# Kernel optimization log

Measured on AMD Instinct MI355X. Metric: run time of the kernel, lower is better.

Reference implementation:

```python
import math
import jax, jax.numpy as jnp
import numpy as np

B, S, H, NH = 4, 2048, 1024, 16
HD = H // NH
SCALE = math.sqrt(H)  # module divides by sqrt(hidden_dim), not sqrt(head_dim)


def setup_inputs() -> dict:
    key = jax.random.key(0)
    ks = jax.random.split(key, 9)
    lim = 1.0 / math.sqrt(H)
    def lin(kw, kb):
        W = jax.random.uniform(kw, (H, H), jnp.float32, -lim, lim)
        b = jax.random.uniform(kb, (H,), jnp.float32, -lim, lim)
        return W, b
    Wq, bq = lin(ks[0], ks[1])
    Wk, bk = lin(ks[2], ks[3])
    Wv, bv = lin(ks[4], ks[5])
    Wo, bo = lin(ks[6], ks[7])
    hidden_states = jax.random.normal(ks[8], (B, S, H), jnp.float32)
    masks = jnp.ones((B, S), jnp.float32)
    return {"hidden_states": hidden_states, "masks": masks,
            "Wq": Wq, "bq": bq, "Wk": Wk, "bk": bk,
            "Wv": Wv, "bv": bv, "Wo": Wo, "bo": bo}


def reference(hidden_states, masks, Wq, bq, Wk, bk, Wv, bv, Wo, bo):
    bsz, msl, hdim = hidden_states.shape
    def proj(W, b):
        # [b, s, h] -> [b, nh, s, hd]
        y = hidden_states @ W.T + b
        return y.reshape(bsz, msl, NH, HD).transpose(0, 2, 1, 3)
    q = proj(Wq, bq)
    k = proj(Wk, bk)
    v = proj(Wv, bv)
    scores = jnp.einsum('bnqd,bnkd->bnqk', q, k) / SCALE
    # mask outer product: [b,1,q,k], zero where either token is padded
    m2 = (masks[:, None, :, None] * masks[:, None, None, :])
    scores = jnp.where(m2 == 0, jnp.float32(-1e12), scores)
    attn = jax.nn.softmax(scores, axis=-1)
    ctx = jnp.einsum('bnqk,bnkd->bnqd', attn, v)
    ctx = ctx.transpose(0, 2, 1, 3).reshape(bsz, msl, hdim)
    return ctx @ Wo.T + bo
```

## Files before the change

kernel.cpp:

```cpp
#include <hip/hip_runtime.h>
#include <hip/hip_bf16.h>
#include <stdint.h>

typedef unsigned short u16;
typedef __attribute__((ext_vector_type(4))) float f32x4;
typedef __attribute__((ext_vector_type(8))) short bf16x8;
typedef __attribute__((ext_vector_type(4))) unsigned int u32x4;

#define GLL16(src, dst) __builtin_amdgcn_global_load_lds( \
    (const __attribute__((address_space(1))) void*)(src), \
    (__attribute__((address_space(3))) void*)(dst), 16, 0, 0)

static __device__ __forceinline__ u16 f2bf(float x) {
    uint32_t u = __builtin_bit_cast(uint32_t, x);
    u += 0x7fffu + ((u >> 16) & 1u);
    return (u16)(u >> 16);
}

static __device__ __forceinline__ uint32_t cvtpk(float lo, float hi) {
    uint32_t r;
    asm("v_cvt_pk_bf16_f32 %0, %1, %2" : "=v"(r) : "v"(lo), "v"(hi));
    return r;
}

__global__ __launch_bounds__(256) void cvt_f32_bf16(
        const float* __restrict__ in, u16* __restrict__ out, int n4) {
    int i = blockIdx.x * 256 + threadIdx.x;
    if (i >= n4) return;
    float4 v = ((const float4*)in)[i];
    ushort4 o;
    o.x = f2bf(v.x); o.y = f2bf(v.y); o.z = f2bf(v.z); o.w = f2bf(v.w);
    ((ushort4*)out)[i] = o;
}

__global__ __launch_bounds__(256) void cvt_w4(
        const float* __restrict__ s0, const float* __restrict__ s1,
        const float* __restrict__ s2, const float* __restrict__ s3,
        u16* __restrict__ dst) {
    int wsel = blockIdx.y;
    const float* s = (wsel == 0) ? s0 : (wsel == 1) ? s1 : (wsel == 2) ? s2 : s3;
    int i = blockIdx.x * 256 + threadIdx.x;
    float4 v = ((const float4*)s)[i];
    ushort4 o;
    o.x = f2bf(v.x); o.y = f2bf(v.y); o.z = f2bf(v.z); o.w = f2bf(v.w);
    ((ushort4*)(dst + (size_t)wsel * 1024 * 1024))[i] = o;
}

__global__ __launch_bounds__(256, 2) void gemm_qkv(
        const u16* __restrict__ A, const u16* __restrict__ W,
        const float* __restrict__ bq, const float* __restrict__ bk,
        const float* __restrict__ bv,
        u16* __restrict__ Qo, u16* __restrict__ Ko, u16* __restrict__ Vo) {
    __shared__ __align__(16) u16 As[2][128 * 32];
    __shared__ __align__(16) u16 Bs[2][128 * 32];
    const int tid = threadIdx.x;
    const int lane = tid & 63;
    const int w = tid >> 6, wm = w >> 1, wn = w & 1;
    const int l15 = lane & 15, l4 = lane >> 4;
    int v = (blockIdx.x & 7) * 192 + (blockIdx.x >> 3);
    int vy = v / 24, vx = v - vy * 24;
    const int m0 = vy * 128, n0 = vx * 128;

    f32x4 acc[4][4];
#pragma unroll
    for (int i = 0; i < 4; i++)
#pragma unroll
        for (int j = 0; j < 4; j++) acc[i][j] = f32x4{0.f, 0.f, 0.f, 0.f};

#define QKV_STAGE(buf, kt) do {                                            \
    _Pragma("unroll")                                                      \
    for (int i_ = 0; i_ < 2; i_++) {                                       \
        int c_ = tid + i_ * 256;                                           \
        int row_ = c_ >> 2, slot_ = c_ & 3;                                \
        int cc_ = slot_ ^ ((row_ >> 1) & 3);                               \
        GLL16(A + (size_t)(m0 + row_) * 1024 + (kt) + cc_ * 8, As[buf] + c_ * 8); \
    }                                                                      \
    _Pragma("unroll")                                                      \
    for (int i_ = 0; i_ < 2; i_++) {                                       \
        int c_ = tid + i_ * 256;                                           \
        int row_ = c_ >> 2, slot_ = c_ & 3;                                \
        int cc_ = slot_ ^ ((row_ >> 1) & 3);                               \
        GLL16(W + (size_t)(n0 + row_) * 1024 + (kt) + cc_ * 8, Bs[buf] + c_ * 8); \
    }                                                                      \
} while (0)

    QKV_STAGE(0, 0);
    __syncthreads();

    for (int kt = 0; kt < 1024; kt += 32) {
        const int cur = (kt >> 5) & 1;
        if (kt != 992) QKV_STAGE(cur ^ 1, kt + 32);

        bf16x8 af[4], bfr[4];
#pragma unroll
        for (int i = 0; i < 4; i++) {
            int row = wm * 64 + i * 16 + l15;
            int slot = l4 ^ ((row >> 1) & 3);
            af[i] = *(const bf16x8*)(As[cur] + row * 32 + slot * 8);
        }
#pragma unroll
        for (int j = 0; j < 4; j++) {
            int row = wn * 64 + j * 16 + l15;
            int slot = l4 ^ ((row >> 1) & 3);
            bfr[j] = *(const bf16x8*)(Bs[cur] + row * 32 + slot * 8);
        }
#pragma unroll
        for (int i = 0; i < 4; i++)
#pragma unroll
            for (int j = 0; j < 4; j++)
                acc[i][j] = __builtin_amdgcn_mfma_f32_16x16x32_bf16(af[i], bfr[j], acc[i][j], 0, 0, 0);
        __syncthreads();
    }
#undef QKV_STAGE

#pragma unroll
    for (int j = 0; j < 4; j++) {
        int col = n0 + wn * 64 + j * 16 + l15;
        int sel = col >> 10;
        float bvv = (sel == 0) ? bq[col] : (sel == 1) ? bk[col - 1024] : bv[col - 2048];
#pragma unroll
        for (int i = 0; i < 4; i++) {
            int rowb = m0 + wm * 64 + i * 16 + l4 * 4;
            if (sel == 0) {
#pragma unroll
                for (int r = 0; r < 4; r++)
                    Qo[(size_t)(rowb + r) * 1024 + col] = f2bf(acc[i][j][r] + bvv);
            } else if (sel == 1) {
#pragma unroll
                for (int r = 0; r < 4; r++)
                    Ko[(size_t)(rowb + r) * 1024 + (col - 1024)] = f2bf(acc[i][j][r] + bvv);
            } else {
                int cc = col - 2048;
                int bb = rowb >> 11;
                int sp = ((m0 + wm * 64) & 2047) + (i >> 1) * 32 + l4 * 8 + (i & 1) * 4;
                int hh = cc >> 6, dd = cc & 63;
                ushort4 o;
                o.x = f2bf(acc[i][j][0] + bvv);
                o.y = f2bf(acc[i][j][1] + bvv);
                o.z = f2bf(acc[i][j][2] + bvv);
                o.w = f2bf(acc[i][j][3] + bvv);
                *(ushort4*)(Vo + ((size_t)((bb * 16 + hh) * 64 + dd)) * 2048 + sp) = o;
            }
        }
    }
}

__global__ __launch_bounds__(256, 2) void gemm_o(
        const u16* __restrict__ A, const u16* __restrict__ W,
        const float* __restrict__ bias, float* __restrict__ out) {
    __shared__ __align__(16) u16 As[2][128 * 32];
    __shared__ __align__(16) u16 Bs[2][128 * 32];
    const int tid = threadIdx.x;
    const int lane = tid & 63;
    const int w = tid >> 6, wm = w >> 1, wn = w & 1;
    const int l15 = lane & 15, l4 = lane >> 4;
    int v = (blockIdx.x & 7) * 64 + (blockIdx.x >> 3);
    int vy = v >> 3, vx = v & 7;
    const int m0 = vy * 128, n0 = vx * 128;

    f32x4 acc[4][4];
#pragma unroll
    for (int i = 0; i < 4; i++)
#pragma unroll
        for (int j = 0; j < 4; j++) acc[i][j] = f32x4{0.f, 0.f, 0.f, 0.f};

#define O_STAGE(buf, kt) do {                                              \
    _Pragma("unroll")                                                      \
    for (int i_ = 0; i_ < 2; i_++) {                                       \
        int c_ = tid + i_ * 256;                                           \
        int row_ = c_ >> 2, slot_ = c_ & 3;                                \
        int cc_ = slot_ ^ ((row_ >> 1) & 3);                               \
        GLL16(A + (size_t)(m0 + row_) * 1024 + (kt) + cc_ * 8, As[buf] + c_ * 8); \
    }                                                                      \
    _Pragma("unroll")                                                      \
    for (int i_ = 0; i_ < 2; i_++) {                                       \
        int c_ = tid + i_ * 256;                                           \
        int row_ = c_ >> 2, slot_ = c_ & 3;                                \
        int cc_ = slot_ ^ ((row_ >> 1) & 3);                               \
        GLL16(W + (size_t)(n0 + row_) * 1024 + (kt) + cc_ * 8, Bs[buf] + c_ * 8); \
    }                                                                      \
} while (0)

    O_STAGE(0, 0);
    __syncthreads();

    for (int kt = 0; kt < 1024; kt += 32) {
        const int cur = (kt >> 5) & 1;
        if (kt != 992) O_STAGE(cur ^ 1, kt + 32);

        bf16x8 af[4], bfr[4];
#pragma unroll
        for (int i = 0; i < 4; i++) {
            int row = wm * 64 + i * 16 + l15;
            int slot = l4 ^ ((row >> 1) & 3);
            af[i] = *(const bf16x8*)(As[cur] + row * 32 + slot * 8);
        }
#pragma unroll
        for (int j = 0; j < 4; j++) {
            int row = wn * 64 + j * 16 + l15;
            int slot = l4 ^ ((row >> 1) & 3);
            bfr[j] = *(const bf16x8*)(Bs[cur] + row * 32 + slot * 8);
        }
#pragma unroll
        for (int i = 0; i < 4; i++)
#pragma unroll
            for (int j = 0; j < 4; j++)
                acc[i][j] = __builtin_amdgcn_mfma_f32_16x16x32_bf16(af[i], bfr[j], acc[i][j], 0, 0, 0);
        __syncthreads();
    }
#undef O_STAGE

#pragma unroll
    for (int j = 0; j < 4; j++) {
        int col = n0 + wn * 64 + j * 16 + l15;
        float bvv = bias[col];
#pragma unroll
        for (int i = 0; i < 4; i++) {
            int rowb = m0 + wm * 64 + i * 16 + l4 * 4;
#pragma unroll
            for (int r = 0; r < 4; r++)
                out[(size_t)(rowb + r) * 1024 + col] = acc[i][j][r] + bvv;
        }
    }
}

__global__ __launch_bounds__(256, 3) void attn_fused(
        const u16* __restrict__ Q, const u16* __restrict__ K,
        const u16* __restrict__ Vt, const float* __restrict__ mask,
        u16* __restrict__ ctx) {
    __shared__ __align__(16) u16 Ks[2][64 * 64];
    __shared__ __align__(16) u16 Vs[2][64 * 64];
    __shared__ int mflag[4];

    const int tid = threadIdx.x, lane = tid & 63, w = tid >> 6;
    const int l15 = lane & 15, l4 = lane >> 4;
    const int bid = blockIdx.x;
    const int inner = bid >> 3;
    const int bh = ((inner >> 4) << 3) | (bid & 7);
    const int b = bh >> 4, h = bh & 15;
    const int qw = (inner & 15) * 128 + w * 32;
    const float SC2 = 0.03125f * 1.44269504088896f;
    const float THR2 = 8.0f;

    const u16* Qg = Q + (size_t)b * 2048 * 1024 + h * 64;
    const u16* Kg = K + (size_t)b * 2048 * 1024 + h * 64;
    const u16* Vg = Vt + (size_t)bh * 64 * 2048;
    const float* mp = mask + b * 2048;

    {
        float4 a = ((const float4*)mp)[tid * 2];
        float4 c = ((const float4*)mp)[tid * 2 + 1];
        bool bad = (a.x == 0.f) | (a.y == 0.f) | (a.z == 0.f) | (a.w == 0.f) |
                   (c.x == 0.f) | (c.y == 0.f) | (c.z == 0.f) | (c.w == 0.f);
        unsigned long long bal = __ballot(bad);
        if (lane == 0) mflag[w] = (bal != 0ull);
    }

    bf16x8 qfr[2][2];
#pragma unroll
    for (int qi = 0; qi < 2; qi++)
#pragma unroll
        for (int kf = 0; kf < 2; kf++)
            qfr[qi][kf] = *(const bf16x8*)(Qg + (size_t)(qw + qi * 16 + l15) * 1024 + kf * 32 + l4 * 8);

    float mqs[2];
#pragma unroll
    for (int qi = 0; qi < 2; qi++)
        mqs[qi] = (mp[qw + qi * 16 + l15] != 0.f) ? SC2 : 0.f;

    __syncthreads();
    const bool anym = (mflag[0] | mflag[1] | mflag[2] | mflag[3]) != 0;

#define STAGE_KV(buf, kvbase) do {                                         \
    _Pragma("unroll")                                                      \
    for (int i_ = 0; i_ < 2; i_++) {                                       \
        int c_ = tid + i_ * 256;                                           \
        int row_ = c_ >> 3, slot_ = c_ & 7;                                \
        int cc_ = slot_ ^ (row_ & 7);                                      \
        GLL16(Kg + (size_t)((kvbase) + row_) * 1024 + cc_ * 8, Ks[buf] + c_ * 8); \
    }                                                                      \
    _Pragma("unroll")                                                      \
    for (int i_ = 0; i_ < 2; i_++) {                                       \
        int c_ = tid + i_ * 256;                                           \
        int row_ = c_ >> 3, slot_ = c_ & 7;                                \
        int cc_ = slot_ ^ (row_ & 7);                                      \
        GLL16(Vg + (size_t)row_ * 2048 + (kvbase) + cc_ * 8, Vs[buf] + c_ * 8); \
    }                                                                      \
} while (0)

    float m_run[2] = {0.f, 0.f};
    f32x4 acc_l[2];
    f32x4 oaccT[4][2];
#pragma unroll
    for (int qi = 0; qi < 2; qi++) acc_l[qi] = f32x4{0.f, 0.f, 0.f, 0.f};
#pragma unroll
    for (int df = 0; df < 4; df++)
#pragma unroll
        for (int qi = 0; qi < 2; qi++) oaccT[df][qi] = f32x4{0.f, 0.f, 0.f, 0.f};

    const u32x4 ones4 = u32x4{0x3F803F80u, 0x3F803F80u, 0x3F803F80u, 0x3F803F80u};
    const bf16x8 ones = __builtin_bit_cast(bf16x8, ones4);

    STAGE_KV(0, 0);
    __syncthreads();

    for (int it = 0; it < 32; ++it) {
        const int cur = it & 1;
        const int kv0 = it * 64;

        if (it != 31) STAGE_KV(cur ^ 1, kv0 + 64);

        bf16x8 kfr[4][2];
#pragma unroll
        for (int kvf = 0; kvf < 4; kvf++)
#pragma unroll
            for (int kf = 0; kf < 2; kf++) {
                int row = kvf * 16 + l15;
                int slot = (kf * 4 + l4) ^ (row & 7);
                kfr[kvf][kf] = *(const bf16x8*)(Ks[cur] + row * 64 + slot * 8);
            }
        f32x4 p[4][2];
#pragma unroll
        for (int kvf = 0; kvf < 4; kvf++)
#pragma unroll
            for (int qi = 0; qi < 2; qi++) p[kvf][qi] = f32x4{0.f, 0.f, 0.f, 0.f};
        __builtin_amdgcn_s_setprio(1);
#pragma unroll
        for (int kvf = 0; kvf < 4; kvf++)
#pragma unroll
            for (int qi = 0; qi < 2; qi++)
#pragma unroll
                for (int kf = 0; kf < 2; kf++)
                    p[kvf][qi] = __builtin_amdgcn_mfma_f32_16x16x32_bf16(kfr[kvf][kf], qfr[qi][kf], p[kvf][qi], 0, 0, 0);
        __builtin_amdgcn_s_setprio(0);

        if (!anym) {
#pragma unroll
            for (int qi = 0; qi < 2; qi++) {
                float mneg = -m_run[qi];
#pragma unroll
                for (int kvf = 0; kvf < 4; kvf++)
#pragma unroll
                    for (int r = 0; r < 4; r++)
                        p[kvf][qi][r] = __builtin_fmaf(p[kvf][qi][r], mqs[qi], mneg);
            }
        } else {
            float4 mkv[4];
#pragma unroll
            for (int kvf = 0; kvf < 4; kvf++)
                mkv[kvf] = ((const float4*)(mp + kv0))[kvf * 4 + l4];
#pragma unroll
            for (int qi = 0; qi < 2; qi++) {
                float mneg = -m_run[qi];
#pragma unroll
                for (int kvf = 0; kvf < 4; kvf++)
#pragma unroll
                    for (int r = 0; r < 4; r++) {
                        float bb = (mkv[kvf][r] != 0.f) ? mneg : -1e12f;
                        p[kvf][qi][r] = __builtin_fmaf(p[kvf][qi][r], mqs[qi], bb);
                    }
            }
        }

        float d2[2];
#pragma unroll
        for (int qi = 0; qi < 2; qi++) {
            float a0 = fmaxf(fmaxf(p[0][qi][0], p[0][qi][1]), fmaxf(p[0][qi][2], p[0][qi][3]));
            float a1 = fmaxf(fmaxf(p[1][qi][0], p[1][qi][1]), fmaxf(p[1][qi][2], p[1][qi][3]));
            float a2 = fmaxf(fmaxf(p[2][qi][0], p[2][qi][1]), fmaxf(p[2][qi][2], p[2][qi][3]));
            float a3 = fmaxf(fmaxf(p[3][qi][0], p[3][qi][1]), fmaxf(p[3][qi][2], p[3][qi][3]));
            float t = fmaxf(fmaxf(a0, a1), fmaxf(a2, a3));
            t = fmaxf(t, __shfl_xor(t, 16));
            t = fmaxf(t, __shfl_xor(t, 32));
            d2[qi] = t;
        }
        if (!__all((d2[0] <= THR2) && (d2[1] <= THR2))) {
#pragma unroll
            for (int qi = 0; qi < 2; qi++) {
                float dd = fmaxf(d2[qi], 0.f);
                float sc = __builtin_amdgcn_exp2f(-dd);
                m_run[qi] += dd;
                acc_l[qi] *= sc;
#pragma unroll
                for (int df = 0; df < 4; df++) oaccT[df][qi] *= sc;
#pragma unroll
                for (int kvf = 0; kvf < 4; kvf++)
#pragma unroll
                    for (int r = 0; r < 4; r++) p[kvf][qi][r] -= dd;
            }
        }
#pragma unroll
        for (int qi = 0; qi < 2; qi++)
#pragma unroll
            for (int kvf = 0; kvf < 4; kvf++)
#pragma unroll
                for (int r = 0; r < 4; r++)
                    p[kvf][qi][r] = __builtin_amdgcn_exp2f(p[kvf][qi][r]);

        bf16x8 pb[2][2];
#pragma unroll
        for (int qi = 0; qi < 2; qi++)
#pragma unroll
            for (int kf = 0; kf < 2; kf++) {
                u32x4 t;
                t.x = cvtpk(p[2 * kf][qi][0], p[2 * kf][qi][1]);
                t.y = cvtpk(p[2 * kf][qi][2], p[2 * kf][qi][3]);
                t.z = cvtpk(p[2 * kf + 1][qi][0], p[2 * kf + 1][qi][1]);
                t.w = cvtpk(p[2 * kf + 1][qi][2], p[2 * kf + 1][qi][3]);
                pb[qi][kf] = __builtin_bit_cast(bf16x8, t);
            }

        bf16x8 vfr[4][2];
#pragma unroll
        for (int df = 0; df < 4; df++)
#pragma unroll
            for (int kf = 0; kf < 2; kf++) {
                int row = df * 16 + l15;
                int slot = (kf * 4 + l4) ^ (row & 7);
                vfr[df][kf] = *(const bf16x8*)(Vs[cur] + row * 64 + slot * 8);
            }

        __builtin_amdgcn_s_setprio(1);
#pragma unroll
        for (int df = 0; df < 4; df++)
#pragma unroll
            for (int qi = 0; qi < 2; qi++)
#pragma unroll
                for (int kf = 0; kf < 2; kf++)
                    oaccT[df][qi] = __builtin_amdgcn_mfma_f32_16x16x32_bf16(vfr[df][kf], pb[qi][kf], oaccT[df][qi], 0, 0, 0);
#pragma unroll
        for (int qi = 0; qi < 2; qi++)
#pragma unroll
            for (int kf = 0; kf < 2; kf++)
                acc_l[qi] = __builtin_amdgcn_mfma_f32_16x16x32_bf16(ones, pb[qi][kf], acc_l[qi], 0, 0, 0);
        __builtin_amdgcn_s_setprio(0);

        __syncthreads();
    }

#pragma unroll
    for (int qi = 0; qi < 2; qi++) {
        float rl = 1.0f / acc_l[qi][0];
        int tok = qw + qi * 16 + l15;
#pragma unroll
        for (int df = 0; df < 4; df++) {
            uint2 o;
            o.x = cvtpk(oaccT[df][qi][0] * rl, oaccT[df][qi][1] * rl);
            o.y = cvtpk(oaccT[df][qi][2] * rl, oaccT[df][qi][3] * rl);
            *(uint2*)(ctx + (size_t)(b * 2048 + tok) * 1024 + h * 64 + df * 16 + l4 * 4) = o;
        }
    }
#undef STAGE_KV
}

extern "C" void kernel_launch(void* const* d_in, const int* in_sizes, int n_in,
                              void* d_out, int out_size, void* d_ws, size_t ws_size,
                              hipStream_t stream) {
    const float* hs    = (const float*)d_in[0];
    const float* masks = (const float*)d_in[1];
    const float* Wq = (const float*)d_in[2];
    const float* bq = (const float*)d_in[3];
    const float* Wk = (const float*)d_in[4];
    const float* bk = (const float*)d_in[5];
    const float* Wv = (const float*)d_in[6];
    const float* bv = (const float*)d_in[7];
    const float* Wo = (const float*)d_in[8];
    const float* bo = (const float*)d_in[9];

    const int NT = 4 * 2048;
    const int H = 1024;

    u16* hs_b = (u16*)d_ws;
    u16* w_b  = hs_b + (size_t)NT * H;
    u16* wo_b = w_b + (size_t)3 * H * H;
    u16* Qb   = w_b + (size_t)4 * H * H;
    u16* Kb   = Qb + (size_t)NT * H;
    u16* Vtb  = Kb + (size_t)NT * H;
    u16* Cb   = hs_b;

    cvt_f32_bf16<<<NT * H / 1024, 256, 0, stream>>>(hs, hs_b, NT * H / 4);
    cvt_w4<<<dim3(H * H / 1024, 4), 256, 0, stream>>>(Wq, Wk, Wv, Wo, w_b);

    gemm_qkv<<<1536, 256, 0, stream>>>(hs_b, w_b, bq, bk, bv, Qb, Kb, Vtb);

    attn_fused<<<1024, 256, 0, stream>>>(Qb, Kb, Vtb, masks, Cb);

    gemm_o<<<512, 256, 0, stream>>>(Cb, wo_b, bo, (float*)d_out);
}
```

Before: 202.4 us.

## Load K/V fragments directly from global memory, dropping LDS staging and barriers

Removes the double-buffered LDS staging of K and V tiles and the per-iteration __syncthreads. Each wave now reads its K and V MFMA fragments straight from global memory, relying on L2 and cache reuse across the four waves. The mask check becomes per-wave with no barrier, and the max-reduction shuffles are deferred into the rare rescale branch. The trade is four times the global/L2 traffic per block, with load latency no longer hidden by an async prefetch of the next tile. The gain is no LDS use, no block-wide syncs and possibly higher occupancy.

```diff
diff --git a/kernel.cpp b/kernel.cpp
--- a/kernel.cpp
+++ b/kernel.cpp
@@ -228,10 +228,6 @@
         const u16* __restrict__ Q, const u16* __restrict__ K,
         const u16* __restrict__ Vt, const float* __restrict__ mask,
         u16* __restrict__ ctx) {
-    __shared__ __align__(16) u16 Ks[2][64 * 64];
-    __shared__ __align__(16) u16 Vs[2][64 * 64];
-    __shared__ int mflag[4];
-
     const int tid = threadIdx.x, lane = tid & 63, w = tid >> 6;
     const int l15 = lane & 15, l4 = lane >> 4;
     const int bid = blockIdx.x;
@@ -247,13 +243,15 @@
     const u16* Vg = Vt + (size_t)bh * 64 * 2048;
     const float* mp = mask + b * 2048;
 
+    bool anym;
     {
-        float4 a = ((const float4*)mp)[tid * 2];
-        float4 c = ((const float4*)mp)[tid * 2 + 1];
-        bool bad = (a.x == 0.f) | (a.y == 0.f) | (a.z == 0.f) | (a.w == 0.f) |
-                   (c.x == 0.f) | (c.y == 0.f) | (c.z == 0.f) | (c.w == 0.f);
-        unsigned long long bal = __ballot(bad);
-        if (lane == 0) mflag[w] = (bal != 0ull);
+        bool bad = false;
+#pragma unroll
+        for (int i = 0; i < 8; i++) {
+            float4 a = ((const float4*)mp)[lane * 8 + i];
+            bad |= (a.x == 0.f) | (a.y == 0.f) | (a.z == 0.f) | (a.w == 0.f);
+        }
+        anym = (__ballot(bad) != 0ull);
     }
 
     bf16x8 qfr[2][2];
@@ -267,26 +265,6 @@
 #pragma unroll
     for (int qi = 0; qi < 2; qi++)
         mqs[qi] = (mp[qw + qi * 16 + l15] != 0.f) ? SC2 : 0.f;
-
-    __syncthreads();
-    const bool anym = (mflag[0] | mflag[1] | mflag[2] | mflag[3]) != 0;
-
-#define STAGE_KV(buf, kvbase) do {                                         \
-    _Pragma("unroll")                                                      \
-    for (int i_ = 0; i_ < 2; i_++) {                                       \
-        int c_ = tid + i_ * 256;                                           \
-        int row_ = c_ >> 3, slot_ = c_ & 7;                                \
-        int cc_ = slot_ ^ (row_ & 7);                                      \
-        GLL16(Kg + (size_t)((kvbase) + row_) * 1024 + cc_ * 8, Ks[buf] + c_ * 8); \
-    }                                                                      \
-    _Pragma("unroll")                                                      \
-    for (int i_ = 0; i_ < 2; i_++) {                                       \
-        int c_ = tid + i_ * 256;                                           \
-        int row_ = c_ >> 3, slot_ = c_ & 7;                                \
-        int cc_ = slot_ ^ (row_ & 7);                                      \
-        GLL16(Vg + (size_t)row_ * 2048 + (kvbase) + cc_ * 8, Vs[buf] + c_ * 8); \
-    }                                                                      \
-} while (0)
 
     float m_run[2] = {0.f, 0.f};
     f32x4 acc_l[2];
@@ -301,24 +279,16 @@
     const u32x4 ones4 = u32x4{0x3F803F80u, 0x3F803F80u, 0x3F803F80u, 0x3F803F80u};
     const bf16x8 ones = __builtin_bit_cast(bf16x8, ones4);
 
-    STAGE_KV(0, 0);
-    __syncthreads();
-
     for (int it = 0; it < 32; ++it) {
-        const int cur = it & 1;
         const int kv0 = it * 64;
 
-        if (it != 31) STAGE_KV(cur ^ 1, kv0 + 64);
-
         bf16x8 kfr[4][2];
 #pragma unroll
         for (int kvf = 0; kvf < 4; kvf++)
 #pragma unroll
-            for (int kf = 0; kf < 2; kf++) {
-                int row = kvf * 16 + l15;
-                int slot = (kf * 4 + l4) ^ (row & 7);
-                kfr[kvf][kf] = *(const bf16x8*)(Ks[cur] + row * 64 + slot * 8);
-            }
+            for (int kf = 0; kf < 2; kf++)
+                kfr[kvf][kf] = *(const bf16x8*)(Kg + (size_t)(kv0 + kvf * 16 + l15) * 1024 + kf * 32 + l4 * 8);
+
         f32x4 p[4][2];
 #pragma unroll
         for (int kvf = 0; kvf < 4; kvf++)
@@ -333,6 +303,13 @@
                 for (int kf = 0; kf < 2; kf++)
                     p[kvf][qi] = __builtin_amdgcn_mfma_f32_16x16x32_bf16(kfr[kvf][kf], qfr[qi][kf], p[kvf][qi], 0, 0, 0);
         __builtin_amdgcn_s_setprio(0);
+
+        bf16x8 vfr[4][2];
+#pragma unroll
+        for (int df = 0; df < 4; df++)
+#pragma unroll
+            for (int kf = 0; kf < 2; kf++)
+                vfr[df][kf] = *(const bf16x8*)(Vg + (size_t)(df * 16 + l15) * 2048 + kv0 + kf * 32 + l4 * 8);
 
         if (!anym) {
 #pragma unroll
@@ -362,22 +339,21 @@
             }
         }
 
-        float d2[2];
+        float t[2];
 #pragma unroll
         for (int qi = 0; qi < 2; qi++) {
             float a0 = fmaxf(fmaxf(p[0][qi][0], p[0][qi][1]), fmaxf(p[0][qi][2], p[0][qi][3]));
             float a1 = fmaxf(fmaxf(p[1][qi][0], p[1][qi][1]), fmaxf(p[1][qi][2], p[1][qi][3]));
             float a2 = fmaxf(fmaxf(p[2][qi][0], p[2][qi][1]), fmaxf(p[2][qi][2], p[2][qi][3]));
             float a3 = fmaxf(fmaxf(p[3][qi][0], p[3][qi][1]), fmaxf(p[3][qi][2], p[3][qi][3]));
-            float t = fmaxf(fmaxf(a0, a1), fmaxf(a2, a3));
-            t = fmaxf(t, __shfl_xor(t, 16));
-            t = fmaxf(t, __shfl_xor(t, 32));
-            d2[qi] = t;
-        }
-        if (!__all((d2[0] <= THR2) && (d2[1] <= THR2))) {
+            t[qi] = fmaxf(fmaxf(a0, a1), fmaxf(a2, a3));
+        }
+        if (!__all((t[0] <= THR2) && (t[1] <= THR2))) {
 #pragma unroll
             for (int qi = 0; qi < 2; qi++) {
-                float dd = fmaxf(d2[qi], 0.f);
+                float tt = fmaxf(t[qi], __shfl_xor(t[qi], 16));
+                tt = fmaxf(tt, __shfl_xor(tt, 32));
+                float dd = fmaxf(tt, 0.f);
                 float sc = __builtin_amdgcn_exp2f(-dd);
                 m_run[qi] += dd;
                 acc_l[qi] *= sc;
@@ -402,22 +378,12 @@
         for (int qi = 0; qi < 2; qi++)
 #pragma unroll
             for (int kf = 0; kf < 2; kf++) {
-                u32x4 t;
-                t.x = cvtpk(p[2 * kf][qi][0], p[2 * kf][qi][1]);
-                t.y = cvtpk(p[2 * kf][qi][2], p[2 * kf][qi][3]);
-                t.z = cvtpk(p[2 * kf + 1][qi][0], p[2 * kf + 1][qi][1]);
-                t.w = cvtpk(p[2 * kf + 1][qi][2], p[2 * kf + 1][qi][3]);
-                pb[qi][kf] = __builtin_bit_cast(bf16x8, t);
-            }
-
-        bf16x8 vfr[4][2];
-#pragma unroll
-        for (int df = 0; df < 4; df++)
-#pragma unroll
-            for (int kf = 0; kf < 2; kf++) {
-                int row = df * 16 + l15;
-                int slot = (kf * 4 + l4) ^ (row & 7);
-                vfr[df][kf] = *(const bf16x8*)(Vs[cur] + row * 64 + slot * 8);
+                u32x4 tq;
+                tq.x = cvtpk(p[2 * kf][qi][0], p[2 * kf][qi][1]);
+                tq.y = cvtpk(p[2 * kf][qi][2], p[2 * kf][qi][3]);
+                tq.z = cvtpk(p[2 * kf + 1][qi][0], p[2 * kf + 1][qi][1]);
+                tq.w = cvtpk(p[2 * kf + 1][qi][2], p[2 * kf + 1][qi][3]);
+                pb[qi][kf] = __builtin_bit_cast(bf16x8, tq);
             }
 
         __builtin_amdgcn_s_setprio(1);
@@ -434,8 +400,6 @@
             for (int kf = 0; kf < 2; kf++)
                 acc_l[qi] = __builtin_amdgcn_mfma_f32_16x16x32_bf16(ones, pb[qi][kf], acc_l[qi], 0, 0, 0);
         __builtin_amdgcn_s_setprio(0);
-
-        __syncthreads();
     }
 
 #pragma unroll
@@ -450,7 +414,6 @@
             *(uint2*)(ctx + (size_t)(b * 2048 + tok) * 1024 + h * 64 + df * 16 + l4 * 4) = o;
         }
     }
-#undef STAGE_KV
 }
 
 extern "C" void kernel_launch(void* const* d_in, const int* in_sizes, int n_in,
```

Result: slower. 392.7 us (+94.0%).

## Fold softmax scale into Q projection and streamline attention max/exp path

Applied to the files above, without the earlier changes.

Moves the 1/sqrt(H)*log2(e) scale into the Q projection epilogue, so the attention kernel skips the per-element FMA when no mask is present. The mask check becomes a per-wave ballot over the whole row, which removes the shared flag array and a block barrier. The online-softmax rescale now tests the per-lane max against the running max before doing any cross-lane shuffles. Exp subtracts the running max only when it is nonzero. This costs an extra subtract on the exp path when rescaling has happened, and Q is now rounded to bf16 after scaling, which slightly changes precision.

```diff
diff --git a/kernel.cpp b/kernel.cpp
--- a/kernel.cpp
+++ b/kernel.cpp
@@ -60,6 +60,7 @@
     int v = (blockIdx.x & 7) * 192 + (blockIdx.x >> 3);
     int vy = v / 24, vx = v - vy * 24;
     const int m0 = vy * 128, n0 = vx * 128;
+    const float SC2 = 0.03125f * 1.44269504088896f;
 
     f32x4 acc[4][4];
 #pragma unroll
@@ -124,7 +125,7 @@
             if (sel == 0) {
 #pragma unroll
                 for (int r = 0; r < 4; r++)
-                    Qo[(size_t)(rowb + r) * 1024 + col] = f2bf(acc[i][j][r] + bvv);
+                    Qo[(size_t)(rowb + r) * 1024 + col] = f2bf((acc[i][j][r] + bvv) * SC2);
             } else if (sel == 1) {
 #pragma unroll
                 for (int r = 0; r < 4; r++)
@@ -230,7 +231,6 @@
         u16* __restrict__ ctx) {
     __shared__ __align__(16) u16 Ks[2][64 * 64];
     __shared__ __align__(16) u16 Vs[2][64 * 64];
-    __shared__ int mflag[4];
 
     const int tid = threadIdx.x, lane = tid & 63, w = tid >> 6;
     const int l15 = lane & 15, l4 = lane >> 4;
@@ -239,7 +239,6 @@
     const int bh = ((inner >> 4) << 3) | (bid & 7);
     const int b = bh >> 4, h = bh & 15;
     const int qw = (inner & 15) * 128 + w * 32;
-    const float SC2 = 0.03125f * 1.44269504088896f;
     const float THR2 = 8.0f;
 
     const u16* Qg = Q + (size_t)b * 2048 * 1024 + h * 64;
@@ -247,29 +246,16 @@
     const u16* Vg = Vt + (size_t)bh * 64 * 2048;
     const float* mp = mask + b * 2048;
 
+    bool anym;
     {
-        float4 a = ((const float4*)mp)[tid * 2];
-        float4 c = ((const float4*)mp)[tid * 2 + 1];
-        bool bad = (a.x == 0.f) | (a.y == 0.f) | (a.z == 0.f) | (a.w == 0.f) |
-                   (c.x == 0.f) | (c.y == 0.f) | (c.z == 0.f) | (c.w == 0.f);
-        unsigned long long bal = __ballot(bad);
-        if (lane == 0) mflag[w] = (bal != 0ull);
-    }
-
-    bf16x8 qfr[2][2];
-#pragma unroll
-    for (int qi = 0; qi < 2; qi++)
-#pragma unroll
-        for (int kf = 0; kf < 2; kf++)
-            qfr[qi][kf] = *(const bf16x8*)(Qg + (size_t)(qw + qi * 16 + l15) * 1024 + kf * 32 + l4 * 8);
-
-    float mqs[2];
-#pragma unroll
-    for (int qi = 0; qi < 2; qi++)
-        mqs[qi] = (mp[qw + qi * 16 + l15] != 0.f) ? SC2 : 0.f;
-
-    __syncthreads();
-    const bool anym = (mflag[0] | mflag[1] | mflag[2] | mflag[3]) != 0;
+        bool bad = false;
+#pragma unroll
+        for (int i = 0; i < 8; i++) {
+            float4 a = ((const float4*)mp)[lane * 8 + i];
+            bad |= (a.x == 0.f) | (a.y == 0.f) | (a.z == 0.f) | (a.w == 0.f);
+        }
+        anym = (__ballot(bad) != 0ull);
+    }
 
 #define STAGE_KV(buf, kvbase) do {                                         \
     _Pragma("unroll")                                                      \
@@ -287,6 +273,18 @@
         GLL16(Vg + (size_t)row_ * 2048 + (kvbase) + cc_ * 8, Vs[buf] + c_ * 8); \
     }                                                                      \
 } while (0)
+
+    bf16x8 qfr[2][2];
+#pragma unroll
+    for (int qi = 0; qi < 2; qi++)
+#pragma unroll
+        for (int kf = 0; kf < 2; kf++)
+            qfr[qi][kf] = *(const bf16x8*)(Qg + (size_t)(qw + qi * 16 + l15) * 1024 + kf * 32 + l4 * 8);
+
+    float mq01[2];
+#pragma unroll
+    for (int qi = 0; qi < 2; qi++)
+        mq01[qi] = (mp[qw + qi * 16 + l15] != 0.f) ? 1.f : 0.f;
 
     float m_run[2] = {0.f, 0.f};
     f32x4 acc_l[2];
@@ -334,80 +332,73 @@
                     p[kvf][qi] = __builtin_amdgcn_mfma_f32_16x16x32_bf16(kfr[kvf][kf], qfr[qi][kf], p[kvf][qi], 0, 0, 0);
         __builtin_amdgcn_s_setprio(0);
 
-        if (!anym) {
-#pragma unroll
-            for (int qi = 0; qi < 2; qi++) {
-                float mneg = -m_run[qi];
-#pragma unroll
-                for (int kvf = 0; kvf < 4; kvf++)
-#pragma unroll
-                    for (int r = 0; r < 4; r++)
-                        p[kvf][qi][r] = __builtin_fmaf(p[kvf][qi][r], mqs[qi], mneg);
-            }
-        } else {
+        if (anym) {
             float4 mkv[4];
 #pragma unroll
             for (int kvf = 0; kvf < 4; kvf++)
                 mkv[kvf] = ((const float4*)(mp + kv0))[kvf * 4 + l4];
 #pragma unroll
-            for (int qi = 0; qi < 2; qi++) {
-                float mneg = -m_run[qi];
+            for (int qi = 0; qi < 2; qi++)
 #pragma unroll
                 for (int kvf = 0; kvf < 4; kvf++)
 #pragma unroll
                     for (int r = 0; r < 4; r++) {
-                        float bb = (mkv[kvf][r] != 0.f) ? mneg : -1e12f;
-                        p[kvf][qi][r] = __builtin_fmaf(p[kvf][qi][r], mqs[qi], bb);
+                        float bb = (mkv[kvf][r] != 0.f) ? 0.f : -1e12f;
+                        p[kvf][qi][r] = __builtin_fmaf(p[kvf][qi][r], mq01[qi], bb);
                     }
-            }
-        }
-
-        float d2[2];
+        }
+
+        float t[2];
 #pragma unroll
         for (int qi = 0; qi < 2; qi++) {
             float a0 = fmaxf(fmaxf(p[0][qi][0], p[0][qi][1]), fmaxf(p[0][qi][2], p[0][qi][3]));
             float a1 = fmaxf(fmaxf(p[1][qi][0], p[1][qi][1]), fmaxf(p[1][qi][2], p[1][qi][3]));
             float a2 = fmaxf(fmaxf(p[2][qi][0], p[2][qi][1]), fmaxf(p[2][qi][2], p[2][qi][3]));
             float a3 = fmaxf(fmaxf(p[3][qi][0], p[3][qi][1]), fmaxf(p[3][qi][2], p[3][qi][3]));
-            float t = fmaxf(fmaxf(a0, a1), fmaxf(a2, a3));
-            t = fmaxf(t, __shfl_xor(t, 16));
-            t = fmaxf(t, __shfl_xor(t, 32));
-            d2[qi] = t;
-        }
-        if (!__all((d2[0] <= THR2) && (d2[1] <= THR2))) {
+            t[qi] = fmaxf(fmaxf(a0, a1), fmaxf(a2, a3));
+        }
+        if (!__all((t[0] <= m_run[0] + THR2) && (t[1] <= m_run[1] + THR2))) {
 #pragma unroll
             for (int qi = 0; qi < 2; qi++) {
-                float dd = fmaxf(d2[qi], 0.f);
-                float sc = __builtin_amdgcn_exp2f(-dd);
-                m_run[qi] += dd;
+                float tt = fmaxf(t[qi], __shfl_xor(t[qi], 16));
+                tt = fmaxf(tt, __shfl_xor(tt, 32));
+                float mn = fmaxf(m_run[qi], tt);
+                float sc = __builtin_amdgcn_exp2f(m_run[qi] - mn);
+                m_run[qi] = mn;
                 acc_l[qi] *= sc;
 #pragma unroll
                 for (int df = 0; df < 4; df++) oaccT[df][qi] *= sc;
+            }
+        }
+        if (__all((m_run[0] == 0.f) & (m_run[1] == 0.f))) {
+#pragma unroll
+            for (int qi = 0; qi < 2; qi++)
 #pragma unroll
                 for (int kvf = 0; kvf < 4; kvf++)
 #pragma unroll
-                    for (int r = 0; r < 4; r++) p[kvf][qi][r] -= dd;
-            }
-        }
+                    for (int r = 0; r < 4; r++)
+                        p[kvf][qi][r] = __builtin_amdgcn_exp2f(p[kvf][qi][r]);
+        } else {
+#pragma unroll
+            for (int qi = 0; qi < 2; qi++)
+#pragma unroll
+                for (int kvf = 0; kvf < 4; kvf++)
+#pragma unroll
+                    for (int r = 0; r < 4; r++)
+                        p[kvf][qi][r] = __builtin_amdgcn_exp2f(p[kvf][qi][r] - m_run[qi]);
+        }
+
+        bf16x8 pb[2][2];
 #pragma unroll
         for (int qi = 0; qi < 2; qi++)
 #pragma unroll
-            for (int kvf = 0; kvf < 4; kvf++)
-#pragma unroll
-                for (int r = 0; r < 4; r++)
-                    p[kvf][qi][r] = __builtin_amdgcn_exp2f(p[kvf][qi][r]);
-
-        bf16x8 pb[2][2];
-#pragma unroll
-        for (int qi = 0; qi < 2; qi++)
-#pragma unroll
             for (int kf = 0; kf < 2; kf++) {
-                u32x4 t;
-                t.x = cvtpk(p[2 * kf][qi][0], p[2 * kf][qi][1]);
-                t.y = cvtpk(p[2 * kf][qi][2], p[2 * kf][qi][3]);
-                t.z = cvtpk(p[2 * kf + 1][qi][0], p[2 * kf + 1][qi][1]);
-                t.w = cvtpk(p[2 * kf + 1][qi][2], p[2 * kf + 1][qi][3]);
-                pb[qi][kf] = __builtin_bit_cast(bf16x8, t);
+                u32x4 tq;
+                tq.x = cvtpk(p[2 * kf][qi][0], p[2 * kf][qi][1]);
+                tq.y = cvtpk(p[2 * kf][qi][2], p[2 * kf][qi][3]);
+                tq.z = cvtpk(p[2 * kf + 1][qi][0], p[2 * kf + 1][qi][1]);
+                tq.w = cvtpk(p[2 * kf + 1][qi][2], p[2 * kf + 1][qi][3]);
+                pb[qi][kf] = __builtin_bit_cast(bf16x8, tq);
             }
 
         bf16x8 vfr[4][2];
```

After: 197.1 us. 1.03x faster.
